# Optimization experiments

Hardware: AMD Instinct MI355X
Metric: run time of the kernel (lower is better)

## Reference

```python
import jax, jax.numpy as jnp
import numpy as np

N_NODES = 50000


def _gcn_conv(x, W, b, edge_index, num_nodes):
    # PyG GCNConv defaults: add self loops, symmetric normalization.
    h = x @ W  # [N, out]
    loop = jnp.arange(num_nodes, dtype=edge_index.dtype)
    src = jnp.concatenate([edge_index[0], loop])  # [E+N]
    dst = jnp.concatenate([edge_index[1], loop])
    ones = jnp.ones(src.shape[0], dtype=x.dtype)
    deg = jax.ops.segment_sum(ones, dst, num_segments=num_nodes)  # in-degree incl. self loop
    dinv = jnp.where(deg > 0, jax.lax.rsqrt(deg), 0.0)
    norm = dinv[src] * dinv[dst]  # [E+N]
    msgs = h[src] * norm[:, None]  # gather + scale (memory-bound)
    out = jax.ops.segment_sum(msgs, dst, num_segments=num_nodes)
    return out + b


def setup_inputs() -> dict:
    key = jax.random.key(0)
    k1, k2, k3, k4 = jax.random.split(key, 4)
    F_in, H = 128, 16
    x = jax.random.normal(k1, (N_NODES, F_in), dtype=jnp.float32)
    edge_index = jax.random.randint(k2, (2, 800000), 0, N_NODES, dtype=jnp.int64)
    # Glorot-ish init for weights
    W1 = jax.random.normal(k3, (F_in, H), dtype=jnp.float32) / np.sqrt(F_in)
    W2 = jax.random.normal(k4, (H, F_in), dtype=jnp.float32) / np.sqrt(H)
    b1 = jnp.zeros((H,), dtype=jnp.float32)
    b2 = jnp.zeros((F_in,), dtype=jnp.float32)
    return {"x": x, "edge_index": edge_index, "W1": W1, "b1": b1, "W2": W2, "b2": b2}


def reference(x, edge_index, W1, b1, W2, b2):
    h = jax.nn.relu(_gcn_conv(x, W1, b1, edge_index, N_NODES))
    out = _gcn_conv(h, W2, b2, edge_index, N_NODES)
    return out
```

## Files before the change

### kernel.cpp

```cpp
#include <hip/hip_runtime.h>

#define N_NODES 50000
#define NPB 128
#define NBUCKET ((N_NODES + NPB - 1) / NPB)
#define CAP 2816
#define CHUNK 4096


__global__ void k_init(int* __restrict__ gcursor) {
    int b = threadIdx.x;
    if (b < NBUCKET) gcursor[b] = b * CAP;
}


__global__ __launch_bounds__(512) void k_part(const int* __restrict__ src,
                                              const int* __restrict__ dst,
                                              int* __restrict__ gcursor,
                                              int* __restrict__ ewords, int E) {
    __shared__ int words[CHUNK];
    __shared__ int hist[512];
    __shared__ int lstart[512];
    __shared__ int gbase[512];

    int tid = threadIdx.x;
    int cbase = blockIdx.x * CHUNK;
    int count = min(CHUNK, E - cbase);

    hist[tid] = 0;
    __syncthreads();

    int w[CHUNK / 512];
#pragma unroll
    for (int r = 0; r < CHUNK / 512; r++) {
        int i = cbase + tid + 512 * r;
        if (i < E) {
            int s = src[i];
            int d = dst[i];
            int b = d >> 7;
            w[r] = s | ((d & 127) << 16) | (b << 23);
            atomicAdd(&hist[b], 1);
        } else {
            w[r] = -1;
        }
    }
    __syncthreads();

    int h = hist[tid];
    for (int off = 1; off < 512; off <<= 1) {
        int t = (tid >= off) ? hist[tid - off] : 0;
        __syncthreads();
        hist[tid] += t;
        __syncthreads();
    }
    int excl = hist[tid] - h;
    __syncthreads();
    hist[tid] = excl;
    lstart[tid] = excl;
    __syncthreads();

#pragma unroll
    for (int r = 0; r < CHUNK / 512; r++) {
        if (w[r] != -1) {
            int b = ((unsigned)w[r]) >> 23;
            int pos = atomicAdd(&hist[b], 1);
            words[pos] = w[r];
        }
    }
    __syncthreads();

    if (tid < NBUCKET) {
        int nb = hist[tid] - lstart[tid];
        gbase[tid] = (nb > 0) ? atomicAdd(&gcursor[tid], nb) : 0;
    }
    __syncthreads();

    for (int i = tid; i < count; i += 512) {
        int ww = words[i];
        int b = ((unsigned)ww) >> 23;
        int g = gbase[b] + (i - lstart[b]);
        ewords[g] = ww;
    }
}


__global__ __launch_bounds__(256) void k_sort(const int* __restrict__ ewords,
                                              const int* __restrict__ gcursor,
                                              unsigned short* __restrict__ eidx,
                                              int* __restrict__ row_start,
                                              int* __restrict__ deg,
                                              float* __restrict__ dinv) {
    __shared__ unsigned short sorted[CAP];
    __shared__ int hist[NPB];
    __shared__ int sc[NPB];
    int tid = threadIdx.x;
    int b = blockIdx.x;
    int base = b * CAP;
    int count = gcursor[b] - base;

    if (tid < NPB) hist[tid] = 0;
    __syncthreads();

    int w[(CAP + 255) / 256];
#pragma unroll
    for (int r = 0; r < (CAP + 255) / 256; r++) {
        int i = tid + 256 * r;
        if (i < count) {
            int ww = ewords[base + i];
            w[r] = ww;
            atomicAdd(&hist[(ww >> 16) & 127], 1);
        } else {
            w[r] = -1;
        }
    }
    __syncthreads();

    int v = 0;
    if (tid < NPB) { v = hist[tid]; sc[tid] = v; }
    __syncthreads();
    for (int off = 1; off < NPB; off <<= 1) {
        int t = 0;
        if (tid < NPB && tid >= off) t = sc[tid - off];
        __syncthreads();
        if (tid < NPB) sc[tid] += t;
        __syncthreads();
    }
    if (tid < NPB) {
        int excl = sc[tid] - v;
        int node = b * NPB + tid;
        if (node < N_NODES) {
            row_start[node] = base + excl;
            deg[node] = v;
            dinv[node] = rsqrtf((float)(v + 1));
        }
        hist[tid] = excl;
    }
    __syncthreads();

#pragma unroll
    for (int r = 0; r < (CAP + 255) / 256; r++) {
        if (w[r] != -1) {
            int ldst = (w[r] >> 16) & 127;
            int pos = atomicAdd(&hist[ldst], 1);
            sorted[pos] = (unsigned short)(w[r] & 0xFFFF);
        }
    }
    __syncthreads();

    for (int i = tid; i < count; i += 256) eidx[base + i] = sorted[i];
}


__global__ __launch_bounds__(256) void k_gemm1(const float* __restrict__ x,
                                               const float* __restrict__ W1,
                                               const float* __restrict__ dinv,
                                               float* __restrict__ h1s) {
    __shared__ float sx[16 * 132];
    __shared__ float swT[16 * 132];
    int tid = threadIdx.x;
    int n0 = blockIdx.x * 16;

#pragma unroll
    for (int r = 0; r < 2; r++) {
        int q = tid + 256 * r;
        float4 v = ((const float4*)W1)[q];
        int k = q >> 2;
        int j4 = (q & 3) << 2;
        swT[(j4 + 0) * 132 + k] = v.x;
        swT[(j4 + 1) * 132 + k] = v.y;
        swT[(j4 + 2) * 132 + k] = v.z;
        swT[(j4 + 3) * 132 + k] = v.w;
    }
    const float4* x4 = (const float4*)(x + (size_t)n0 * 128);
#pragma unroll
    for (int r = 0; r < 2; r++) {
        int q = tid + 256 * r;
        float4 v = x4[q];
        int node = q >> 5;
        int k = (q & 31) << 2;
        *(float4*)&sx[node * 132 + k] = v;
    }
    __syncthreads();

    int node = tid >> 4;
    int j = tid & 15;
    float acc = 0.f;
#pragma unroll
    for (int k = 0; k < 128; k += 4) {
        float4 a = *(const float4*)&sx[node * 132 + k];
        float4 bb = *(const float4*)&swT[j * 132 + k];
        acc = fmaf(a.x, bb.x, acc);
        acc = fmaf(a.y, bb.y, acc);
        acc = fmaf(a.z, bb.z, acc);
        acc = fmaf(a.w, bb.w, acc);
    }
    int n = n0 + node;
    h1s[(size_t)n * 16 + j] = dinv[n] * acc;
}


__global__ __launch_bounds__(256) void k_agg(const float* __restrict__ hin,
                                             const int* __restrict__ row_start,
                                             const int* __restrict__ deg,
                                             const unsigned short* __restrict__ eidx,
                                             const float* __restrict__ dinv,
                                             const float* __restrict__ bias,
                                             float* __restrict__ hout, int mode) {
    int lane = threadIdx.x & 63;
    int node = blockIdx.x * 4 + (threadIdx.x >> 6);
    int f = lane & 15;
    int sub = lane >> 4;

    int start = row_start[node];
    int d = deg[node];

    float a0 = 0.f, a1 = 0.f;
    int i = sub;
    for (; i + 4 < d; i += 8) {
        int s0 = eidx[start + i];
        int s1 = eidx[start + i + 4];
        a0 += hin[s0 * 16 + f];
        a1 += hin[s1 * 16 + f];
    }
    if (i < d) a0 += hin[(int)eidx[start + i] * 16 + f];
    float acc = a0 + a1;

    acc += __shfl_xor(acc, 16, 64);
    acc += __shfl_xor(acc, 32, 64);
    acc += hin[node * 16 + f];

    float dv = dinv[node];
    float v;
    if (mode == 0) {
        v = fmaxf(dv * acc + bias[f], 0.f) * dv;
    } else {
        v = dv * acc;
    }
    if (sub == 0) hout[node * 16 + f] = v;
}


__global__ __launch_bounds__(256) void k_gemm2(const float* __restrict__ s2,
                                               const float* __restrict__ W2,
                                               const float* __restrict__ b2,
                                               float* __restrict__ out) {
    __shared__ float sw2[16 * 128];
    __shared__ float ss2[16 * 16];
    int tid = threadIdx.x;
    int n0 = blockIdx.x * 16;

    ((float4*)sw2)[tid] = ((const float4*)W2)[tid];
    ((float4*)sw2)[tid + 256] = ((const float4*)W2)[tid + 256];
    if (tid < 64) ((float4*)ss2)[tid] = ((const float4*)(s2 + (size_t)n0 * 16))[tid];
    __syncthreads();

    int j = tid & 127;
    int half = tid >> 7;
    float w[16];
#pragma unroll
    for (int k = 0; k < 16; k++) w[k] = sw2[k * 128 + j];
    float bj = b2[j];

#pragma unroll
    for (int r = 0; r < 8; r++) {
        int node = half + r * 2;
        float acc2 = bj;
#pragma unroll
        for (int k = 0; k < 16; k++) acc2 = fmaf(ss2[node * 16 + k], w[k], acc2);
        out[(size_t)(n0 + node) * 128 + j] = acc2;
    }
}


extern "C" void kernel_launch(void* const* d_in, const int* in_sizes, int n_in,
                              void* d_out, int out_size, void* d_ws, size_t ws_size,
                              hipStream_t stream) {
    const float* x  = (const float*)d_in[0];
    const int*   ei = (const int*)d_in[1];
    const float* W1 = (const float*)d_in[2];
    const float* b1 = (const float*)d_in[3];
    const float* W2 = (const float*)d_in[4];
    const float* b2 = (const float*)d_in[5];
    float* out = (float*)d_out;

    const int E = in_sizes[1] / 2;
    const int* src = ei;
    const int* dst = ei + E;

    char* ws = (char*)d_ws;
    int*            gcursor   = (int*)(ws + 0);
    int*            ewords    = (int*)(ws + 2048);
    float*          h1s       = (float*)(ws + 2048);
    float*          s2        = h1s;
    unsigned short* eidx      = (unsigned short*)(ws + 4406272);
    int*            row_start = (int*)(ws + 6608384);
    int*            deg       = (int*)(ws + 6808384);
    float*          dinv      = (float*)(ws + 7008384);
    float*          z1s       = (float*)(ws + 7208384);

    const int NCHUNK = (E + CHUNK - 1) / CHUNK;

    k_init<<<1, 512, 0, stream>>>(gcursor);
    k_part<<<NCHUNK, 512, 0, stream>>>(src, dst, gcursor, ewords, E);
    k_sort<<<NBUCKET, 256, 0, stream>>>(ewords, gcursor, eidx, row_start, deg, dinv);
    k_gemm1<<<N_NODES / 16, 256, 0, stream>>>(x, W1, dinv, h1s);
    k_agg<<<N_NODES / 4, 256, 0, stream>>>(h1s, row_start, deg, eidx, dinv, b1, z1s, 0);
    k_agg<<<N_NODES / 4, 256, 0, stream>>>(z1s, row_start, deg, eidx, dinv, b2, s2, 1);
    k_gemm2<<<N_NODES / 16, 256, 0, stream>>>(s2, W2, b2, out);
}
```

Before: 157.3 us.

## Fuse sort with gemm1 and agg2 with gemm2, shuffle-scan partitioning

Runs the bucket sort and the first dense GEMM side by side in one launch by splitting the grid, which means h1 is no longer pre-scaled by dinv. The first aggregation therefore gathers dinv per neighbor instead. The second aggregation is fused with the 16x128 output GEMM through wave shuffles, removing the intermediate s2 round trip and one launch. Partitioning now uses smaller chunks with int4 loads, a wave-shuffle scan and a memset in place of the init kernel. The trade-offs are an extra dinv gather per edge and a serial 16-node loop per wave in the fused kernel, which may lower parallelism.

Measured after the change: 169.5 us. 1.08x slower.

```diff
diff --git a/kernel.cpp b/kernel.cpp
--- a/kernel.cpp
+++ b/kernel.cpp
@@ -4,13 +4,8 @@
 #define NPB 128
 #define NBUCKET ((N_NODES + NPB - 1) / NPB)
 #define CAP 2816
-#define CHUNK 4096
-
-
-__global__ void k_init(int* __restrict__ gcursor) {
-    int b = threadIdx.x;
-    if (b < NBUCKET) gcursor[b] = b * CAP;
-}
+#define CHUNK 2048
+#define EPT 4
 
 
 __global__ __launch_bounds__(512) void k_part(const int* __restrict__ src,
@@ -21,6 +16,7 @@
     __shared__ int hist[512];
     __shared__ int lstart[512];
     __shared__ int gbase[512];
+    __shared__ int wsum[8];
 
     int tid = threadIdx.x;
     int cbase = blockIdx.x * CHUNK;
@@ -29,37 +25,55 @@
     hist[tid] = 0;
     __syncthreads();
 
-    int w[CHUNK / 512];
-#pragma unroll
-    for (int r = 0; r < CHUNK / 512; r++) {
-        int i = cbase + tid + 512 * r;
-        if (i < E) {
-            int s = src[i];
-            int d = dst[i];
-            int b = d >> 7;
-            w[r] = s | ((d & 127) << 16) | (b << 23);
+    int w[EPT];
+    if (cbase + CHUNK <= E) {
+        int4 s4 = ((const int4*)(src + cbase))[tid];
+        int4 d4 = ((const int4*)(dst + cbase))[tid];
+        int ss[EPT] = {s4.x, s4.y, s4.z, s4.w};
+        int dd[EPT] = {d4.x, d4.y, d4.z, d4.w};
+#pragma unroll
+        for (int r = 0; r < EPT; r++) {
+            int b = dd[r] >> 7;
+            w[r] = ss[r] | ((dd[r] & 127) << 16) | (b << 23);
             atomicAdd(&hist[b], 1);
-        } else {
-            w[r] = -1;
+        }
+    } else {
+#pragma unroll
+        for (int r = 0; r < EPT; r++) {
+            int i = tid * EPT + r;
+            if (i < count) {
+                int s = src[cbase + i];
+                int d = dst[cbase + i];
+                int b = d >> 7;
+                w[r] = s | ((d & 127) << 16) | (b << 23);
+                atomicAdd(&hist[b], 1);
+            } else {
+                w[r] = -1;
+            }
         }
     }
     __syncthreads();
 
     int h = hist[tid];
-    for (int off = 1; off < 512; off <<= 1) {
-        int t = (tid >= off) ? hist[tid - off] : 0;
-        __syncthreads();
-        hist[tid] += t;
-        __syncthreads();
-    }
-    int excl = hist[tid] - h;
-    __syncthreads();
+    int lane = tid & 63;
+    int v = h;
+#pragma unroll
+    for (int off = 1; off < 64; off <<= 1) {
+        int t = __shfl_up(v, off, 64);
+        if (lane >= off) v += t;
+    }
+    if (lane == 63) wsum[tid >> 6] = v;
+    __syncthreads();
+    int woff = 0;
+    int wv = tid >> 6;
+    for (int i = 0; i < wv; i++) woff += wsum[i];
+    int excl = v + woff - h;
     hist[tid] = excl;
     lstart[tid] = excl;
     __syncthreads();
 
 #pragma unroll
-    for (int r = 0; r < CHUNK / 512; r++) {
+    for (int r = 0; r < EPT; r++) {
         if (w[r] != -1) {
             int b = ((unsigned)w[r]) >> 23;
             int pos = atomicAdd(&hist[b], 1);
@@ -77,134 +91,133 @@
     for (int i = tid; i < count; i += 512) {
         int ww = words[i];
         int b = ((unsigned)ww) >> 23;
-        int g = gbase[b] + (i - lstart[b]);
-        ewords[g] = ww;
-    }
-}
-
-
-__global__ __launch_bounds__(256) void k_sort(const int* __restrict__ ewords,
-                                              const int* __restrict__ gcursor,
-                                              unsigned short* __restrict__ eidx,
-                                              int* __restrict__ row_start,
-                                              int* __restrict__ deg,
-                                              float* __restrict__ dinv) {
-    __shared__ unsigned short sorted[CAP];
-    __shared__ int hist[NPB];
-    __shared__ int sc[NPB];
+        ewords[b * CAP + gbase[b] + (i - lstart[b])] = ww;
+    }
+}
+
+
+__global__ __launch_bounds__(256) void k_sortgemm1(const int* __restrict__ ewords,
+                                                   const int* __restrict__ gcursor,
+                                                   unsigned short* __restrict__ eidx,
+                                                   int* __restrict__ row_start,
+                                                   int* __restrict__ deg,
+                                                   float* __restrict__ dinv,
+                                                   const float* __restrict__ x,
+                                                   const float* __restrict__ W1,
+                                                   float* __restrict__ h1) {
+    __shared__ __align__(16) char smem[16 * 132 * 4 * 2];
     int tid = threadIdx.x;
-    int b = blockIdx.x;
-    int base = b * CAP;
-    int count = gcursor[b] - base;
-
-    if (tid < NPB) hist[tid] = 0;
-    __syncthreads();
-
-    int w[(CAP + 255) / 256];
-#pragma unroll
-    for (int r = 0; r < (CAP + 255) / 256; r++) {
-        int i = tid + 256 * r;
-        if (i < count) {
-            int ww = ewords[base + i];
-            w[r] = ww;
-            atomicAdd(&hist[(ww >> 16) & 127], 1);
-        } else {
-            w[r] = -1;
-        }
-    }
-    __syncthreads();
-
-    int v = 0;
-    if (tid < NPB) { v = hist[tid]; sc[tid] = v; }
-    __syncthreads();
-    for (int off = 1; off < NPB; off <<= 1) {
-        int t = 0;
-        if (tid < NPB && tid >= off) t = sc[tid - off];
-        __syncthreads();
-        if (tid < NPB) sc[tid] += t;
-        __syncthreads();
-    }
-    if (tid < NPB) {
-        int excl = sc[tid] - v;
-        int node = b * NPB + tid;
-        if (node < N_NODES) {
-            row_start[node] = base + excl;
-            deg[node] = v;
-            dinv[node] = rsqrtf((float)(v + 1));
-        }
-        hist[tid] = excl;
-    }
-    __syncthreads();
-
-#pragma unroll
-    for (int r = 0; r < (CAP + 255) / 256; r++) {
-        if (w[r] != -1) {
-            int ldst = (w[r] >> 16) & 127;
-            int pos = atomicAdd(&hist[ldst], 1);
-            sorted[pos] = (unsigned short)(w[r] & 0xFFFF);
-        }
-    }
-    __syncthreads();
-
-    for (int i = tid; i < count; i += 256) eidx[base + i] = sorted[i];
-}
-
-
-__global__ __launch_bounds__(256) void k_gemm1(const float* __restrict__ x,
-                                               const float* __restrict__ W1,
-                                               const float* __restrict__ dinv,
-                                               float* __restrict__ h1s) {
-    __shared__ float sx[16 * 132];
-    __shared__ float swT[16 * 132];
-    int tid = threadIdx.x;
-    int n0 = blockIdx.x * 16;
-
-#pragma unroll
-    for (int r = 0; r < 2; r++) {
-        int q = tid + 256 * r;
-        float4 v = ((const float4*)W1)[q];
-        int k = q >> 2;
-        int j4 = (q & 3) << 2;
-        swT[(j4 + 0) * 132 + k] = v.x;
-        swT[(j4 + 1) * 132 + k] = v.y;
-        swT[(j4 + 2) * 132 + k] = v.z;
-        swT[(j4 + 3) * 132 + k] = v.w;
-    }
-    const float4* x4 = (const float4*)(x + (size_t)n0 * 128);
-#pragma unroll
-    for (int r = 0; r < 2; r++) {
-        int q = tid + 256 * r;
-        float4 v = x4[q];
-        int node = q >> 5;
-        int k = (q & 31) << 2;
-        *(float4*)&sx[node * 132 + k] = v;
-    }
-    __syncthreads();
-
-    int node = tid >> 4;
-    int j = tid & 15;
-    float acc = 0.f;
-#pragma unroll
-    for (int k = 0; k < 128; k += 4) {
-        float4 a = *(const float4*)&sx[node * 132 + k];
-        float4 bb = *(const float4*)&swT[j * 132 + k];
-        acc = fmaf(a.x, bb.x, acc);
-        acc = fmaf(a.y, bb.y, acc);
-        acc = fmaf(a.z, bb.z, acc);
-        acc = fmaf(a.w, bb.w, acc);
-    }
-    int n = n0 + node;
-    h1s[(size_t)n * 16 + j] = dinv[n] * acc;
-}
-
-
-__global__ __launch_bounds__(256) void k_agg(const float* __restrict__ hin,
-                                             const int* __restrict__ row_start,
-                                             const int* __restrict__ deg,
-                                             const unsigned short* __restrict__ eidx,
-                                             const float* __restrict__ dinv,
-                                             const float* __restrict__ bias,
-                                             float* __restrict__ hout, int mode) {
+
+    if (blockIdx.x < NBUCKET) {
+        unsigned short* sorted = (unsigned short*)smem;
+        int* hist = (int*)(smem + 5632);
+        int* sc   = (int*)(smem + 5632 + 512);
+
+        int b = blockIdx.x;
+        int base = b * CAP;
+        int count = gcursor[b];
+
+        if (tid < NPB) hist[tid] = 0;
+        __syncthreads();
+
+        int w[(CAP + 255) / 256];
+#pragma unroll
+        for (int r = 0; r < (CAP + 255) / 256; r++) {
+            int i = tid + 256 * r;
+            if (i < count) {
+                int ww = ewords[base + i];
+                w[r] = ww;
+                atomicAdd(&hist[(ww >> 16) & 127], 1);
+            } else {
+                w[r] = -1;
+            }
+        }
+        __syncthreads();
+
+        int v = 0;
+        if (tid < NPB) { v = hist[tid]; sc[tid] = v; }
+        __syncthreads();
+        for (int off = 1; off < NPB; off <<= 1) {
+            int t = 0;
+            if (tid < NPB && tid >= off) t = sc[tid - off];
+            __syncthreads();
+            if (tid < NPB) sc[tid] += t;
+            __syncthreads();
+        }
+        if (tid < NPB) {
+            int excl = sc[tid] - v;
+            int node = b * NPB + tid;
+            if (node < N_NODES) {
+                row_start[node] = base + excl;
+                deg[node] = v;
+                dinv[node] = rsqrtf((float)(v + 1));
+            }
+            hist[tid] = excl;
+        }
+        __syncthreads();
+
+#pragma unroll
+        for (int r = 0; r < (CAP + 255) / 256; r++) {
+            if (w[r] != -1) {
+                int ldst = (w[r] >> 16) & 127;
+                int pos = atomicAdd(&hist[ldst], 1);
+                sorted[pos] = (unsigned short)(w[r] & 0xFFFF);
+            }
+        }
+        __syncthreads();
+
+        for (int i = tid; i < count; i += 256) eidx[base + i] = sorted[i];
+    } else {
+        float* sx  = (float*)smem;
+        float* swT = sx + 16 * 132;
+        int n0 = (blockIdx.x - NBUCKET) * 16;
+
+#pragma unroll
+        for (int r = 0; r < 2; r++) {
+            int q = tid + 256 * r;
+            float4 v = ((const float4*)W1)[q];
+            int k = q >> 2;
+            int j4 = (q & 3) << 2;
+            swT[(j4 + 0) * 132 + k] = v.x;
+            swT[(j4 + 1) * 132 + k] = v.y;
+            swT[(j4 + 2) * 132 + k] = v.z;
+            swT[(j4 + 3) * 132 + k] = v.w;
+        }
+        const float4* x4 = (const float4*)(x + (size_t)n0 * 128);
+#pragma unroll
+        for (int r = 0; r < 2; r++) {
+            int q = tid + 256 * r;
+            float4 v = x4[q];
+            int node = q >> 5;
+            int k = (q & 31) << 2;
+            *(float4*)&sx[node * 132 + k] = v;
+        }
+        __syncthreads();
+
+        int node = tid >> 4;
+        int j = tid & 15;
+        float acc = 0.f;
+#pragma unroll
+        for (int k = 0; k < 128; k += 4) {
+            float4 a = *(const float4*)&sx[node * 132 + k];
+            float4 bb = *(const float4*)&swT[j * 132 + k];
+            acc = fmaf(a.x, bb.x, acc);
+            acc = fmaf(a.y, bb.y, acc);
+            acc = fmaf(a.z, bb.z, acc);
+            acc = fmaf(a.w, bb.w, acc);
+        }
+        h1[(size_t)(n0 + node) * 16 + j] = acc;
+    }
+}
+
+
+__global__ __launch_bounds__(256) void k_agg1(const float* __restrict__ h1,
+                                              const int* __restrict__ row_start,
+                                              const int* __restrict__ deg,
+                                              const unsigned short* __restrict__ eidx,
+                                              const float* __restrict__ dinv,
+                                              const float* __restrict__ b1,
+                                              float* __restrict__ z1s) {
     int lane = threadIdx.x & 63;
     int node = blockIdx.x * 4 + (threadIdx.x >> 6);
     int f = lane & 15;
@@ -218,55 +231,84 @@
     for (; i + 4 < d; i += 8) {
         int s0 = eidx[start + i];
         int s1 = eidx[start + i + 4];
-        a0 += hin[s0 * 16 + f];
-        a1 += hin[s1 * 16 + f];
-    }
-    if (i < d) a0 += hin[(int)eidx[start + i] * 16 + f];
+        float d0 = dinv[s0];
+        float d1 = dinv[s1];
+        a0 = fmaf(d0, h1[s0 * 16 + f], a0);
+        a1 = fmaf(d1, h1[s1 * 16 + f], a1);
+    }
+    if (i < d) {
+        int s = eidx[start + i];
+        a0 = fmaf(dinv[s], h1[s * 16 + f], a0);
+    }
     float acc = a0 + a1;
 
     acc += __shfl_xor(acc, 16, 64);
     acc += __shfl_xor(acc, 32, 64);
-    acc += hin[node * 16 + f];
 
     float dv = dinv[node];
-    float v;
-    if (mode == 0) {
-        v = fmaxf(dv * acc + bias[f], 0.f) * dv;
-    } else {
-        v = dv * acc;
-    }
-    if (sub == 0) hout[node * 16 + f] = v;
-}
-
-
-__global__ __launch_bounds__(256) void k_gemm2(const float* __restrict__ s2,
+    acc = fmaf(dv, h1[node * 16 + f], acc);
+    float z = fmaxf(fmaf(dv, acc, b1[f]), 0.f);
+    if (sub == 0) z1s[node * 16 + f] = dv * z;
+}
+
+
+__global__ __launch_bounds__(256) void k_aggmm(const float* __restrict__ z1s,
+                                               const int* __restrict__ row_start,
+                                               const int* __restrict__ deg,
+                                               const unsigned short* __restrict__ eidx,
+                                               const float* __restrict__ dinv,
                                                const float* __restrict__ W2,
                                                const float* __restrict__ b2,
                                                float* __restrict__ out) {
     __shared__ float sw2[16 * 128];
-    __shared__ float ss2[16 * 16];
+    __shared__ float sb2[128];
     int tid = threadIdx.x;
-    int n0 = blockIdx.x * 16;
 
     ((float4*)sw2)[tid] = ((const float4*)W2)[tid];
     ((float4*)sw2)[tid + 256] = ((const float4*)W2)[tid + 256];
-    if (tid < 64) ((float4*)ss2)[tid] = ((const float4*)(s2 + (size_t)n0 * 16))[tid];
-    __syncthreads();
-
-    int j = tid & 127;
-    int half = tid >> 7;
-    float w[16];
-#pragma unroll
-    for (int k = 0; k < 16; k++) w[k] = sw2[k * 128 + j];
-    float bj = b2[j];
-
-#pragma unroll
-    for (int r = 0; r < 8; r++) {
-        int node = half + r * 2;
-        float acc2 = bj;
-#pragma unroll
-        for (int k = 0; k < 16; k++) acc2 = fmaf(ss2[node * 16 + k], w[k], acc2);
-        out[(size_t)(n0 + node) * 128 + j] = acc2;
+    if (tid < 32) ((float4*)sb2)[tid] = ((const float4*)b2)[tid];
+    __syncthreads();
+
+    int wave = tid >> 6;
+    int lane = tid & 63;
+    int f = lane & 15;
+    int sub = lane >> 4;
+    int nbase = (blockIdx.x * 4 + wave) * 16;
+
+#pragma unroll 1
+    for (int t = 0; t < 16; t++) {
+        int node = nbase + t;
+        if (node >= N_NODES) break;
+
+        int start = row_start[node];
+        int d = deg[node];
+
+        float a0 = 0.f, a1 = 0.f;
+        int i = sub;
+        for (; i + 4 < d; i += 8) {
+            int s0 = eidx[start + i];
+            int s1 = eidx[start + i + 4];
+            a0 += z1s[s0 * 16 + f];
+            a1 += z1s[s1 * 16 + f];
+        }
+        if (i < d) a0 += z1s[(int)eidx[start + i] * 16 + f];
+        float acc = a0 + a1;
+
+        acc += __shfl_xor(acc, 16, 64);
+        acc += __shfl_xor(acc, 32, 64);
+        acc += z1s[node * 16 + f];
+        float s2 = dinv[node] * acc;
+
+        float o0 = sb2[lane];
+        float o1 = sb2[lane + 64];
+#pragma unroll
+        for (int k = 0; k < 16; k++) {
+            float sk = __shfl(s2, k, 64);
+            o0 = fmaf(sk, sw2[k * 128 + lane], o0);
+            o1 = fmaf(sk, sw2[k * 128 + 64 + lane], o1);
+        }
+        out[(size_t)node * 128 + lane] = o0;
+        out[(size_t)node * 128 + 64 + lane] = o1;
     }
 }
 
@@ -289,21 +331,20 @@
     char* ws = (char*)d_ws;
     int*            gcursor   = (int*)(ws + 0);
     int*            ewords    = (int*)(ws + 2048);
-    float*          h1s       = (float*)(ws + 2048);
-    float*          s2        = h1s;
-    unsigned short* eidx      = (unsigned short*)(ws + 4406272);
-    int*            row_start = (int*)(ws + 6608384);
-    int*            deg       = (int*)(ws + 6808384);
-    float*          dinv      = (float*)(ws + 7008384);
-    float*          z1s       = (float*)(ws + 7208384);
+    float*          h1        = (float*)(ws + 4406272);
+    unsigned short* eidx      = (unsigned short*)(ws + 7606272);
+    int*            row_start = (int*)(ws + 9808384);
+    int*            deg       = (int*)(ws + 10008384);
+    float*          dinv      = (float*)(ws + 10208384);
+    float*          z1s       = (float*)(ws + 10408384);
 
     const int NCHUNK = (E + CHUNK - 1) / CHUNK;
 
-    k_init<<<1, 512, 0, stream>>>(gcursor);
+    hipMemsetAsync(gcursor, 0, NBUCKET * sizeof(int), stream);
     k_part<<<NCHUNK, 512, 0, stream>>>(src, dst, gcursor, ewords, E);
-    k_sort<<<NBUCKET, 256, 0, stream>>>(ewords, gcursor, eidx, row_start, deg, dinv);
-    k_gemm1<<<N_NODES / 16, 256, 0, stream>>>(x, W1, dinv, h1s);
-    k_agg<<<N_NODES / 4, 256, 0, stream>>>(h1s, row_start, deg, eidx, dinv, b1, z1s, 0);
-    k_agg<<<N_NODES / 4, 256, 0, stream>>>(z1s, row_start, deg, eidx, dinv, b2, s2, 1);
-    k_gemm2<<<N_NODES / 16, 256, 0, stream>>>(s2, W2, b2, out);
-}
+    k_sortgemm1<<<NBUCKET + N_NODES / 16, 256, 0, stream>>>(ewords, gcursor, eidx,
+                                                            row_start, deg, dinv, x, W1, h1);
+    k_agg1<<<N_NODES / 4, 256, 0, stream>>>(h1, row_start, deg, eidx, dinv, b1, z1s);
+    k_aggmm<<<(N_NODES + 63) / 64, 256, 0, stream>>>(z1s, row_start, deg, eidx, dinv,
+                                                     W2, b2, out);
+}
```
